# Kernel optimization log

Measured on AMD Instinct MI355X. Metric: run time of the kernel, lower is better.

The kernel has to match this reference:

```python
import jax, jax.numpy as jnp
import numpy as np

D_MODEL = 1024
N_HEADS = 16
D_K = D_MODEL // N_HEADS


def setup_inputs() -> dict:
    key = jax.random.key(0)
    ks = jax.random.split(key, 9)
    B, L = 2, 2048
    s = 1.0 / np.sqrt(D_MODEL)
    return {
        "x": jax.random.normal(ks[0], (B, L, D_MODEL), dtype=jnp.float32),
        "Wq": jax.random.normal(ks[1], (D_MODEL, D_MODEL), dtype=jnp.float32) * s,
        "bq": jnp.zeros((D_MODEL,), dtype=jnp.float32),
        "Wk": jax.random.normal(ks[2], (D_MODEL, D_MODEL), dtype=jnp.float32) * s,
        "bk": jnp.zeros((D_MODEL,), dtype=jnp.float32),
        "Wv": jax.random.normal(ks[3], (D_MODEL, D_MODEL), dtype=jnp.float32) * s,
        "bv": jnp.zeros((D_MODEL,), dtype=jnp.float32),
        "Wo": jax.random.normal(ks[4], (D_MODEL, D_MODEL), dtype=jnp.float32) * s,
        "bo": jnp.zeros((D_MODEL,), dtype=jnp.float32),
    }


def reference(x, Wq, bq, Wk, bk, Wv, bv, Wo, bo):
    B, L, D = x.shape
    H, dk = N_HEADS, D_K
    # torch Linear: y = x @ W.T + b
    def proj(W, b):
        y = jnp.einsum('bld,ed->ble', x, W) + b
        return y.reshape(B, L, H, dk).transpose(0, 2, 1, 3)  # [B,H,L,dk]
    Q = proj(Wq, bq)
    K = proj(Wk, bk)
    V = proj(Wv, bv)
    scores = jnp.einsum('bhqd,bhkd->bhqk', Q, K) / jnp.sqrt(jnp.float32(dk))
    probs = jax.nn.softmax(scores, axis=-1)
    # intervention: zero column 0, then average with original -> halve column 0
    col_scale = jnp.where(jnp.arange(L) == 0, 0.5, 1.0).astype(probs.dtype)
    combined = probs * col_scale  # broadcast over last axis
    out = jnp.einsum('bhqk,bhkd->bhqd', combined, V)
    out = out.transpose(0, 2, 1, 3).reshape(B, L, D)
    # dropout in eval mode = identity
    return jnp.einsum('bld,ed->ble', out, Wo) + bo
```

## Files before the change

kernel.cpp:

```cpp
#include <hip/hip_runtime.h>
#include <stdint.h>

#define DMODEL 1024
#define LSEQ   2048
#define NBATCH 2
#define NHEADS 16
#define DKH    64
#define MROWS  4096
#define KSPLIT 2

typedef __attribute__((ext_vector_type(8))) short short8;
typedef __attribute__((ext_vector_type(4))) float f32x4;
typedef __attribute__((ext_vector_type(16))) float f32x16;
typedef __attribute__((ext_vector_type(2))) int int2v;

__device__ __forceinline__ unsigned short f2b(float f) {
  union { float f; unsigned int u; } v; v.f = f;
  unsigned int r = v.u + 0x7FFFu + ((v.u >> 16) & 1u);
  return (unsigned short)(r >> 16);
}

__device__ __forceinline__ float b2f(unsigned short u) {
  union { unsigned int i; float f; } v; v.i = ((unsigned int)u) << 16; return v.f;
}

__device__ __forceinline__ unsigned int cvtpk(float lo, float hi) {
  unsigned int r;
  asm volatile("v_cvt_pk_bf16_f32 %0, %1, %2" : "=v"(r) : "v"(lo), "v"(hi));
  return r;
}

__device__ __forceinline__ int2v pl32swap(unsigned int a, unsigned int b) {
  return __builtin_amdgcn_permlane32_swap((int)a, (int)b, false, false);
}

__device__ __forceinline__ void async16(const void* g, void* l) {
  __builtin_amdgcn_global_load_lds(
      (const __attribute__((address_space(1))) unsigned int*)g,
      (__attribute__((address_space(3))) unsigned int*)l, 16, 0, 0);
}

__global__ void k_cvt(const float* __restrict__ s, unsigned short* __restrict__ d, int n4) {
  int i = blockIdx.x * blockDim.x + threadIdx.x;
  if (i >= n4) return;
  float4 v = ((const float4*)s)[i];
  ushort4 o;
  o.x = f2b(v.x); o.y = f2b(v.y); o.z = f2b(v.z); o.w = f2b(v.w);
  ((ushort4*)d)[i] = o;
}

__global__ void k_cvtw(const float* __restrict__ s0, const float* __restrict__ s1,
                       const float* __restrict__ s2, const float* __restrict__ s3,
                       unsigned short* __restrict__ d0, unsigned short* __restrict__ d1,
                       unsigned short* __restrict__ d2, unsigned short* __restrict__ d3) {
  const float* s; unsigned short* d;
  switch (blockIdx.y) {
    case 0: s = s0; d = d0; break;
    case 1: s = s1; d = d1; break;
    case 2: s = s2; d = d2; break;
    default: s = s3; d = d3; break;
  }
  int i = blockIdx.x * blockDim.x + threadIdx.x;
  float4 v = ((const float4*)s)[i];
  ushort4 o;
  o.x = f2b(v.x); o.y = f2b(v.y); o.z = f2b(v.z); o.w = f2b(v.w);
  ((ushort4*)d)[i] = o;
}

__device__ __forceinline__ void gemm_mainloop(
    const unsigned short* __restrict__ A, const unsigned short* __restrict__ B,
    int rowBase, int colBase, char* As, char* Bs, f32x4 acc[4][4])
{
  const int tid  = threadIdx.x;
  const int lane = tid & 63;
  const int wr   = tid >> 7;
  const int wc   = (tid >> 6) & 1;
  for (int kt = 0; kt < DMODEL / 64; ++kt) {
    const int k0 = kt * 64;
    __syncthreads();
#pragma unroll
    for (int p = 0; p < 4; ++p) {
      const int chunk = p * 256 + tid;
      const int row   = chunk >> 3;
      const int cs    = (chunk & 7) ^ (row & 7);
      async16(A + (size_t)(rowBase + row) * DMODEL + k0 + cs * 8,
              As + (p * 256 + (tid & 0xC0)) * 16);
      async16(B + (size_t)(colBase + row) * DMODEL + k0 + cs * 8,
              Bs + (p * 256 + (tid & 0xC0)) * 16);
    }
    __syncthreads();
#pragma unroll
    for (int ks = 0; ks < 2; ++ks) {
      short8 af[4], bfr[4];
#pragma unroll
      for (int m = 0; m < 4; ++m) {
        const int ra = wr * 64 + m * 16 + (lane & 15);
        af[m]  = *(const short8*)(As + ra * 128 + (((ks * 4 + (lane >> 4)) ^ (ra & 7)) * 16));
        const int rb = wc * 64 + m * 16 + (lane & 15);
        bfr[m] = *(const short8*)(Bs + rb * 128 + (((ks * 4 + (lane >> 4)) ^ (rb & 7)) * 16));
      }
#pragma unroll
      for (int m = 0; m < 4; ++m)
#pragma unroll
        for (int n = 0; n < 4; ++n)
          acc[m][n] = __builtin_amdgcn_mfma_f32_16x16x32_bf16(af[m], bfr[n], acc[m][n], 0, 0, 0);
    }
  }
}

__global__ __launch_bounds__(256, 2) void k_gemm_qkv(
    const unsigned short* __restrict__ xb,
    const unsigned short* __restrict__ Wqb, const unsigned short* __restrict__ Wkb,
    const unsigned short* __restrict__ Wvb,
    const float* __restrict__ bq, const float* __restrict__ bk, const float* __restrict__ bv,
    unsigned short* __restrict__ Q, unsigned short* __restrict__ Ksw,
    unsigned short* __restrict__ Vsw)
{
  __shared__ char As[16384];
  __shared__ char Bs[16384];
  const int z = blockIdx.z;
  const unsigned short* W = (z == 0) ? Wqb : ((z == 1) ? Wkb : Wvb);
  const float* bias       = (z == 0) ? bq  : ((z == 1) ? bk  : bv);
  const int rowBase = blockIdx.x * 128, colBase = blockIdx.y * 128;

  f32x4 zero = {0.f, 0.f, 0.f, 0.f};
  f32x4 acc[4][4];
#pragma unroll
  for (int m = 0; m < 4; ++m)
#pragma unroll
    for (int n = 0; n < 4; ++n) acc[m][n] = zero;

  gemm_mainloop(xb, W, rowBase, colBase, As, Bs, acc);

  const int tid = threadIdx.x, lane = tid & 63;
  const int wr = tid >> 7, wc = (tid >> 6) & 1;
  const float scale = (z == 0) ? 0.18033688011112042f : 1.0f;
#pragma unroll
  for (int m = 0; m < 4; ++m) {
#pragma unroll
    for (int n = 0; n < 4; ++n) {
      const int gcol = colBase + wc * 64 + n * 16 + (lane & 15);
      const float bb = bias[gcol];
      const int h = gcol >> 6, d = gcol & 63;
      if (z == 0) {
#pragma unroll
        for (int r = 0; r < 4; ++r) {
          const int grow = rowBase + wr * 64 + m * 16 + ((lane >> 4) << 2) + r;
          const int bi = grow >> 11, l = grow & 2047;
          Q[(((size_t)(bi * NHEADS + h)) * LSEQ + l) * DKH + d] =
              f2b((acc[m][n][r] + bb) * scale);
        }
      } else if (z == 1) {
#pragma unroll
        for (int r = 0; r < 4; ++r) {
          const int grow = rowBase + wr * 64 + m * 16 + ((lane >> 4) << 2) + r;
          const int bi = grow >> 11, l = grow & 2047;
          const int bh = bi * NHEADS + h;
          Ksw[(size_t)(bh * 32 + (l >> 6)) * 4096 + ((d >> 3) * 64 + (l & 63)) * 8 + (d & 7)] =
              f2b(acc[m][n][r] + bb);
        }
      } else {
        const int grow0 = rowBase + wr * 64 + m * 16 + ((lane >> 4) << 2);
        const int bi = grow0 >> 11, l0 = grow0 & 2047;
        const int bh = bi * NHEADS + h;
        ushort4 o;
        o.x = f2b(acc[m][n][0] + bb);
        o.y = f2b(acc[m][n][1] + bb);
        o.z = f2b(acc[m][n][2] + bb);
        o.w = f2b(acc[m][n][3] + bb);
        *(ushort4*)(Vsw + (size_t)(bh * 32 + (l0 >> 6)) * 4096 +
                    (((l0 & 63) >> 3) * 64 + d) * 8 + (l0 & 7)) = o;
      }
    }
  }
}

__global__ __launch_bounds__(256, 4) void k_attn(
    const unsigned short* __restrict__ Q, const unsigned short* __restrict__ Ksw,
    const unsigned short* __restrict__ Vsw,
    unsigned short* __restrict__ Op0, unsigned short* __restrict__ Op1,
    float* __restrict__ Lp)
{
  __shared__ char Ks[2][8192];
  __shared__ char Vs[2][8192];

  const int tid = threadIdx.x, lane = tid & 63, w = tid >> 6;
  const int hi = lane >> 5;
  const int ql = lane & 31;

  const int flat = blockIdx.x;
  const int g  = flat & 63;
  const int qi = flat >> 6;
  const int bh = g >> 1, ks = g & 1;
  const int b = bh >> 4, h = bh & 15;
  const int q0 = qi * 128 + w * 32;

  unsigned short* __restrict__ Op = ks ? Op1 : Op0;
  const unsigned short* __restrict__ Qh = Q + (size_t)bh * LSEQ * DKH;

  short8 qf[4];
#pragma unroll
  for (int c = 0; c < 4; ++c)
    qf[c] = *(const short8*)(Qh + (size_t)(q0 + ql) * DKH + c * 16 + hi * 8);

  union { unsigned short u[8]; short8 v; } ones;
#pragma unroll
  for (int j = 0; j < 8; ++j) ones.u[j] = 0x3F80;

  f32x16 oacc[2], lacc, z16;
#pragma unroll
  for (int r = 0; r < 16; ++r) {
    oacc[0][r] = 0.f; oacc[1][r] = 0.f; lacc[r] = 0.f; z16[r] = 0.f;
  }
  float p0 = 0.f;

  auto stage = [&](int buf, int kt2) {
    const unsigned short* Kt = Ksw + (size_t)(bh * 32 + kt2) * 4096;
    const unsigned short* Vt = Vsw + (size_t)(bh * 32 + kt2) * 4096;
#pragma unroll
    for (int p = 0; p < 2; ++p) {
      const int c = p * 256 + tid;
      async16(Kt + c * 8, Ks[buf] + (p * 256 + (tid & 0xC0)) * 16);
      async16(Vt + c * 8, Vs[buf] + (p * 256 + (tid & 0xC0)) * 16);
    }
  };

  const int t0 = ks * (LSEQ / 64 / KSPLIT);
  const int NT = LSEQ / 64 / KSPLIT;

  stage(0, t0);
  __syncthreads();

  int cur = 0;
  for (int it = 0; it < NT; ++it) {
    if (it < NT - 1) stage(cur ^ 1, t0 + it + 1);
    const char* Kc = Ks[cur];
    const char* Vc = Vs[cur];

    f32x16 sv[2];
#pragma unroll
    for (int b2 = 0; b2 < 2; ++b2) {
      short8 kf = *(const short8*)(Kc + ((0 * 2 + hi) * 64 + b2 * 32 + ql) * 16);
      sv[b2] = __builtin_amdgcn_mfma_f32_32x32x16_bf16(kf, qf[0], z16, 0, 0, 0);
    }
#pragma unroll
    for (int c = 1; c < 4; ++c) {
#pragma unroll
      for (int b2 = 0; b2 < 2; ++b2) {
        short8 kf = *(const short8*)(Kc + ((c * 2 + hi) * 64 + b2 * 32 + ql) * 16);
        sv[b2] = __builtin_amdgcn_mfma_f32_32x32x16_bf16(kf, qf[c], sv[b2], 0, 0, 0);
      }
    }

#pragma unroll
    for (int b2 = 0; b2 < 2; ++b2)
#pragma unroll
      for (int r = 0; r < 16; ++r) sv[b2][r] = __builtin_amdgcn_exp2f(sv[b2][r]);

    if (ks == 0 && it == 0 && hi == 0) { p0 = sv[0][0]; sv[0][0] *= 0.5f; }

    unsigned int pk[2][4][2];
#pragma unroll
    for (int b2 = 0; b2 < 2; ++b2)
#pragma unroll
      for (int R = 0; R < 4; ++R) {
        pk[b2][R][0] = cvtpk(sv[b2][4 * R + 0], sv[b2][4 * R + 1]);
        pk[b2][R][1] = cvtpk(sv[b2][4 * R + 2], sv[b2][4 * R + 3]);
      }

#pragma unroll
    for (int kc = 0; kc < 4; ++kc) {
      const int b2 = kc >> 1, Rl = 2 * (kc & 1);
      int2v sw0 = pl32swap(pk[b2][Rl][0], pk[b2][Rl + 1][0]);
      int2v sw1 = pl32swap(pk[b2][Rl][1], pk[b2][Rl + 1][1]);
      union { int i[4]; short8 v; } pa;
      pa.i[0] = sw0[0]; pa.i[1] = sw1[0]; pa.i[2] = sw0[1]; pa.i[3] = sw1[1];
      lacc = __builtin_amdgcn_mfma_f32_32x32x16_bf16(pa.v, ones.v, lacc, 0, 0, 0);
#pragma unroll
      for (int n = 0; n < 2; ++n) {
        short8 vb = *(const short8*)(Vc + ((kc * 2 + hi) * 64 + n * 32 + ql) * 16);
        oacc[n] = __builtin_amdgcn_mfma_f32_32x32x16_bf16(pa.v, vb, oacc[n], 0, 0, 0);
      }
    }

    __syncthreads();
    cur ^= 1;
  }

#pragma unroll
  for (int r = 0; r < 16; ++r) {
    const int qrow = (r & 3) + 8 * (r >> 2) + 4 * hi;
    float lv = lacc[r];
    if (ks == 0) lv += 0.5f * __shfl(p0, qrow);
#pragma unroll
    for (int n = 0; n < 2; ++n) {
      Op[(size_t)(b * LSEQ + q0 + qrow) * DMODEL + h * 64 + n * 32 + ql] =
          f2b(oacc[n][r]);
    }
    if (ql == 0)
      Lp[ks * (32 * LSEQ) + bh * LSEQ + q0 + qrow] = lv;
  }
}

__global__ void k_combine(const unsigned short* __restrict__ o0,
                          const unsigned short* __restrict__ o1,
                          const float* __restrict__ Lp,
                          unsigned short* __restrict__ AO)
{
  const int i = blockIdx.x * blockDim.x + threadIdx.x;
  const int row = i >> 7;
  const int q = row & 2047, b = row >> 11;
  const int h = (i & 127) >> 3;
  const int bhq = (b * 16 + h) * 2048 + q;
  const float inv = 1.0f / (Lp[bhq] + Lp[32 * LSEQ + bhq]);
  short8 a = ((const short8*)o0)[i];
  short8 c = ((const short8*)o1)[i];
  union { unsigned short u[8]; short8 v; } o;
#pragma unroll
  for (int j = 0; j < 8; ++j)
    o.u[j] = f2b((b2f((unsigned short)a[j]) + b2f((unsigned short)c[j])) * inv);
  ((short8*)AO)[i] = o.v;
}

__global__ __launch_bounds__(256, 2) void k_gemm_out(
    const unsigned short* __restrict__ AO, const unsigned short* __restrict__ Wob,
    const float* __restrict__ bo, float* __restrict__ out)
{
  __shared__ char As[16384];
  __shared__ char Bs[16384];
  const int rowBase = blockIdx.x * 128, colBase = blockIdx.y * 128;
  f32x4 zero = {0.f, 0.f, 0.f, 0.f};
  f32x4 acc[4][4];
#pragma unroll
  for (int m = 0; m < 4; ++m)
#pragma unroll
    for (int n = 0; n < 4; ++n) acc[m][n] = zero;

  gemm_mainloop(AO, Wob, rowBase, colBase, As, Bs, acc);

  const int tid = threadIdx.x, lane = tid & 63;
  const int wr = tid >> 7, wc = (tid >> 6) & 1;
#pragma unroll
  for (int m = 0; m < 4; ++m) {
#pragma unroll
    for (int n = 0; n < 4; ++n) {
      const int gcol = colBase + wc * 64 + n * 16 + (lane & 15);
      const float bb = bo[gcol];
#pragma unroll
      for (int r = 0; r < 4; ++r) {
        const int grow = rowBase + wr * 64 + m * 16 + ((lane >> 4) << 2) + r;
        out[(size_t)grow * DMODEL + gcol] = acc[m][n][r] + bb;
      }
    }
  }
}

extern "C" void kernel_launch(void* const* d_in, const int* in_sizes, int n_in,
                              void* d_out, int out_size, void* d_ws, size_t ws_size,
                              hipStream_t stream) {
  const float* x  = (const float*)d_in[0];
  const float* Wq = (const float*)d_in[1];
  const float* bq = (const float*)d_in[2];
  const float* Wk = (const float*)d_in[3];
  const float* bk = (const float*)d_in[4];
  const float* Wv = (const float*)d_in[5];
  const float* bv = (const float*)d_in[6];
  const float* Wo = (const float*)d_in[7];
  const float* bo = (const float*)d_in[8];
  float* out = (float*)d_out;
  char* ws = (char*)d_ws;

  const size_t MB = 1u << 20;
  unsigned short* xb  = (unsigned short*)(ws);
  unsigned short* Wob = (unsigned short*)(ws + 8  * MB);
  unsigned short* Wqb = (unsigned short*)(ws + 10 * MB);
  unsigned short* Wkb = (unsigned short*)(ws + 12 * MB);
  unsigned short* Wvb = (unsigned short*)(ws + 14 * MB);
  unsigned short* Qb  = (unsigned short*)(ws + 16 * MB);
  unsigned short* Ksw = (unsigned short*)(ws + 24 * MB);
  unsigned short* Vsw = (unsigned short*)(ws + 32 * MB);
  unsigned short* AOb = (unsigned short*)(ws + 40 * MB);
  unsigned short* Op0 = (unsigned short*)(ws);
  unsigned short* Op1 = (unsigned short*)(ws + 48 * MB);
  float*          Lpp = (float*)(ws + 56 * MB);

  k_cvt<<<4096, 256, 0, stream>>>(x, xb, MROWS * DMODEL / 4);
  dim3 gw(DMODEL * DMODEL / 4 / 256, 4);
  k_cvtw<<<gw, 256, 0, stream>>>(Wq, Wk, Wv, Wo, Wqb, Wkb, Wvb, Wob);

  dim3 gqkv(MROWS / 128, DMODEL / 128, 3);
  k_gemm_qkv<<<gqkv, 256, 0, stream>>>(xb, Wqb, Wkb, Wvb, bq, bk, bv, Qb, Ksw, Vsw);

  k_attn<<<16 * 32 * KSPLIT, 256, 0, stream>>>(Qb, Ksw, Vsw, Op0, Op1, Lpp);

  k_combine<<<2048, 256, 0, stream>>>(Op0, Op1, Lpp, AOb);

  dim3 gout(MROWS / 128, DMODEL / 128);
  k_gemm_out<<<gout, 256, 0, stream>>>(AOb, Wob, bo, out);
}
```

Baseline: 117.7 us.

## Software-pipeline attention: overlap QK^T of next tile with PV of previous tile

The attention loop is restructured so each iteration computes scores for tile i while running the P·V and row-sum MFMAs for tile i-1, with V held in a triple buffer and K in a double buffer. The aim is to hide the exp and convert/permlane latency behind independent MFMA work. The x and weight fp32-to-bf16 conversions are also merged into one launch to save a kernel launch. In exchange the kernel keeps more registers live (the packed probabilities) and uses extra LDS for the third V buffer, which may reduce occupancy.

Result: no change. 115.6 us (-1.8%).

```diff
diff --git a/kernel.cpp b/kernel.cpp
--- a/kernel.cpp
+++ b/kernel.cpp
@@ -40,27 +40,23 @@
       (__attribute__((address_space(3))) unsigned int*)l, 16, 0, 0);
 }
 
-__global__ void k_cvt(const float* __restrict__ s, unsigned short* __restrict__ d, int n4) {
-  int i = blockIdx.x * blockDim.x + threadIdx.x;
-  if (i >= n4) return;
-  float4 v = ((const float4*)s)[i];
-  ushort4 o;
-  o.x = f2b(v.x); o.y = f2b(v.y); o.z = f2b(v.z); o.w = f2b(v.w);
-  ((ushort4*)d)[i] = o;
-}
-
-__global__ void k_cvtw(const float* __restrict__ s0, const float* __restrict__ s1,
-                       const float* __restrict__ s2, const float* __restrict__ s3,
-                       unsigned short* __restrict__ d0, unsigned short* __restrict__ d1,
-                       unsigned short* __restrict__ d2, unsigned short* __restrict__ d3) {
+__global__ void k_cvtall(const float* __restrict__ x,
+                         const float* __restrict__ w0, const float* __restrict__ w1,
+                         const float* __restrict__ w2, const float* __restrict__ w3,
+                         unsigned short* __restrict__ xb,
+                         unsigned short* __restrict__ d0, unsigned short* __restrict__ d1,
+                         unsigned short* __restrict__ d2, unsigned short* __restrict__ d3) {
+  const int y = blockIdx.y;
   const float* s; unsigned short* d;
-  switch (blockIdx.y) {
-    case 0: s = s0; d = d0; break;
-    case 1: s = s1; d = d1; break;
-    case 2: s = s2; d = d2; break;
-    default: s = s3; d = d3; break;
-  }
-  int i = blockIdx.x * blockDim.x + threadIdx.x;
+  switch (y) {
+    case 0: case 1: case 2: case 3:
+      s = x + (size_t)y * 1048576; d = xb + (size_t)y * 1048576; break;
+    case 4: s = w0; d = d0; break;
+    case 5: s = w1; d = d1; break;
+    case 6: s = w2; d = d2; break;
+    default: s = w3; d = d3; break;
+  }
+  const int i = blockIdx.x * blockDim.x + threadIdx.x;
   float4 v = ((const float4*)s)[i];
   ushort4 o;
   o.x = f2b(v.x); o.y = f2b(v.y); o.z = f2b(v.z); o.w = f2b(v.w);
@@ -182,11 +178,12 @@
     float* __restrict__ Lp)
 {
   __shared__ char Ks[2][8192];
-  __shared__ char Vs[2][8192];
-
-  const int tid = threadIdx.x, lane = tid & 63, w = tid >> 6;
+  __shared__ char Vs[3][8192];
+
+  const int tid = threadIdx.x, lane = tid & 63;
   const int hi = lane >> 5;
   const int ql = lane & 31;
+  const int w = tid >> 6;
 
   const int flat = blockIdx.x;
   const int g  = flat & 63;
@@ -214,51 +211,47 @@
   }
   float p0 = 0.f;
 
-  auto stage = [&](int buf, int kt2) {
-    const unsigned short* Kt = Ksw + (size_t)(bh * 32 + kt2) * 4096;
-    const unsigned short* Vt = Vsw + (size_t)(bh * 32 + kt2) * 4096;
+  auto stageK = [&](int slot, int t2) {
+    const unsigned short* Kt = Ksw + (size_t)(bh * 32 + t2) * 4096;
 #pragma unroll
     for (int p = 0; p < 2; ++p) {
       const int c = p * 256 + tid;
-      async16(Kt + c * 8, Ks[buf] + (p * 256 + (tid & 0xC0)) * 16);
-      async16(Vt + c * 8, Vs[buf] + (p * 256 + (tid & 0xC0)) * 16);
+      async16(Kt + c * 8, Ks[slot] + (p * 256 + (tid & 0xC0)) * 16);
+    }
+  };
+  auto stageV = [&](int slot, int t2) {
+    const unsigned short* Vt = Vsw + (size_t)(bh * 32 + t2) * 4096;
+#pragma unroll
+    for (int p = 0; p < 2; ++p) {
+      const int c = p * 256 + tid;
+      async16(Vt + c * 8, Vs[slot] + (p * 256 + (tid & 0xC0)) * 16);
     }
   };
 
   const int t0 = ks * (LSEQ / 64 / KSPLIT);
   const int NT = LSEQ / 64 / KSPLIT;
 
-  stage(0, t0);
+  stageK(0, t0); stageV(0, t0);
   __syncthreads();
 
-  int cur = 0;
-  for (int it = 0; it < NT; ++it) {
-    if (it < NT - 1) stage(cur ^ 1, t0 + it + 1);
-    const char* Kc = Ks[cur];
-    const char* Vc = Vs[cur];
-
+  short8 paP[4];
+
+  {
+    stageK(1, t0 + 1); stageV(1, t0 + 1);
+    const char* Kc = Ks[0];
     f32x16 sv[2];
 #pragma unroll
-    for (int b2 = 0; b2 < 2; ++b2) {
-      short8 kf = *(const short8*)(Kc + ((0 * 2 + hi) * 64 + b2 * 32 + ql) * 16);
-      sv[b2] = __builtin_amdgcn_mfma_f32_32x32x16_bf16(kf, qf[0], z16, 0, 0, 0);
-    }
-#pragma unroll
-    for (int c = 1; c < 4; ++c) {
-#pragma unroll
-      for (int b2 = 0; b2 < 2; ++b2) {
-        short8 kf = *(const short8*)(Kc + ((c * 2 + hi) * 64 + b2 * 32 + ql) * 16);
-        sv[b2] = __builtin_amdgcn_mfma_f32_32x32x16_bf16(kf, qf[c], sv[b2], 0, 0, 0);
-      }
-    }
-
+    for (int c = 0; c < 4; ++c) {
+      short8 kf0 = *(const short8*)(Kc + ((c * 2 + hi) * 64 + ql) * 16);
+      short8 kf1 = *(const short8*)(Kc + ((c * 2 + hi) * 64 + 32 + ql) * 16);
+      sv[0] = __builtin_amdgcn_mfma_f32_32x32x16_bf16(kf0, qf[c], c ? sv[0] : z16, 0, 0, 0);
+      sv[1] = __builtin_amdgcn_mfma_f32_32x32x16_bf16(kf1, qf[c], c ? sv[1] : z16, 0, 0, 0);
+    }
 #pragma unroll
     for (int b2 = 0; b2 < 2; ++b2)
 #pragma unroll
       for (int r = 0; r < 16; ++r) sv[b2][r] = __builtin_amdgcn_exp2f(sv[b2][r]);
-
-    if (ks == 0 && it == 0 && hi == 0) { p0 = sv[0][0]; sv[0][0] *= 0.5f; }
-
+    if (ks == 0 && hi == 0) { p0 = sv[0][0]; sv[0][0] *= 0.5f; }
     unsigned int pk[2][4][2];
 #pragma unroll
     for (int b2 = 0; b2 < 2; ++b2)
@@ -267,7 +260,6 @@
         pk[b2][R][0] = cvtpk(sv[b2][4 * R + 0], sv[b2][4 * R + 1]);
         pk[b2][R][1] = cvtpk(sv[b2][4 * R + 2], sv[b2][4 * R + 3]);
       }
-
 #pragma unroll
     for (int kc = 0; kc < 4; ++kc) {
       const int b2 = kc >> 1, Rl = 2 * (kc & 1);
@@ -275,16 +267,64 @@
       int2v sw1 = pl32swap(pk[b2][Rl][1], pk[b2][Rl + 1][1]);
       union { int i[4]; short8 v; } pa;
       pa.i[0] = sw0[0]; pa.i[1] = sw1[0]; pa.i[2] = sw0[1]; pa.i[3] = sw1[1];
-      lacc = __builtin_amdgcn_mfma_f32_32x32x16_bf16(pa.v, ones.v, lacc, 0, 0, 0);
-#pragma unroll
-      for (int n = 0; n < 2; ++n) {
-        short8 vb = *(const short8*)(Vc + ((kc * 2 + hi) * 64 + n * 32 + ql) * 16);
-        oacc[n] = __builtin_amdgcn_mfma_f32_32x32x16_bf16(pa.v, vb, oacc[n], 0, 0, 0);
+      paP[kc] = pa.v;
+    }
+    __syncthreads();
+  }
+
+  for (int i = 1; i < NT; ++i) {
+    if (i < NT - 1) { stageK((i + 1) & 1, t0 + i + 1); stageV((i + 1) % 3, t0 + i + 1); }
+    const char* Kc = Ks[i & 1];
+    const char* Vp = Vs[(i - 1) % 3];
+
+    f32x16 sv[2];
+#pragma unroll
+    for (int s = 0; s < 4; ++s) {
+      short8 kf0 = *(const short8*)(Kc + ((s * 2 + hi) * 64 + ql) * 16);
+      short8 kf1 = *(const short8*)(Kc + ((s * 2 + hi) * 64 + 32 + ql) * 16);
+      sv[0] = __builtin_amdgcn_mfma_f32_32x32x16_bf16(kf0, qf[s], s ? sv[0] : z16, 0, 0, 0);
+      sv[1] = __builtin_amdgcn_mfma_f32_32x32x16_bf16(kf1, qf[s], s ? sv[1] : z16, 0, 0, 0);
+      lacc = __builtin_amdgcn_mfma_f32_32x32x16_bf16(paP[s], ones.v, lacc, 0, 0, 0);
+      short8 vb0 = *(const short8*)(Vp + ((s * 2 + hi) * 64 + ql) * 16);
+      short8 vb1 = *(const short8*)(Vp + ((s * 2 + hi) * 64 + 32 + ql) * 16);
+      oacc[0] = __builtin_amdgcn_mfma_f32_32x32x16_bf16(paP[s], vb0, oacc[0], 0, 0, 0);
+      oacc[1] = __builtin_amdgcn_mfma_f32_32x32x16_bf16(paP[s], vb1, oacc[1], 0, 0, 0);
+    }
+
+#pragma unroll
+    for (int b2 = 0; b2 < 2; ++b2)
+#pragma unroll
+      for (int r = 0; r < 16; ++r) sv[b2][r] = __builtin_amdgcn_exp2f(sv[b2][r]);
+    unsigned int pk[2][4][2];
+#pragma unroll
+    for (int b2 = 0; b2 < 2; ++b2)
+#pragma unroll
+      for (int R = 0; R < 4; ++R) {
+        pk[b2][R][0] = cvtpk(sv[b2][4 * R + 0], sv[b2][4 * R + 1]);
+        pk[b2][R][1] = cvtpk(sv[b2][4 * R + 2], sv[b2][4 * R + 3]);
       }
-    }
-
+#pragma unroll
+    for (int kc = 0; kc < 4; ++kc) {
+      const int b2 = kc >> 1, Rl = 2 * (kc & 1);
+      int2v sw0 = pl32swap(pk[b2][Rl][0], pk[b2][Rl + 1][0]);
+      int2v sw1 = pl32swap(pk[b2][Rl][1], pk[b2][Rl + 1][1]);
+      union { int i[4]; short8 v; } pa;
+      pa.i[0] = sw0[0]; pa.i[1] = sw1[0]; pa.i[2] = sw0[1]; pa.i[3] = sw1[1];
+      paP[kc] = pa.v;
+    }
     __syncthreads();
-    cur ^= 1;
+  }
+
+  {
+    const char* Vp = Vs[(NT - 1) % 3];
+#pragma unroll
+    for (int s = 0; s < 4; ++s) {
+      lacc = __builtin_amdgcn_mfma_f32_32x32x16_bf16(paP[s], ones.v, lacc, 0, 0, 0);
+      short8 vb0 = *(const short8*)(Vp + ((s * 2 + hi) * 64 + ql) * 16);
+      short8 vb1 = *(const short8*)(Vp + ((s * 2 + hi) * 64 + 32 + ql) * 16);
+      oacc[0] = __builtin_amdgcn_mfma_f32_32x32x16_bf16(paP[s], vb0, oacc[0], 0, 0, 0);
+      oacc[1] = __builtin_amdgcn_mfma_f32_32x32x16_bf16(paP[s], vb1, oacc[1], 0, 0, 0);
+    }
   }
 
 #pragma unroll
@@ -384,9 +424,8 @@
   unsigned short* Op1 = (unsigned short*)(ws + 48 * MB);
   float*          Lpp = (float*)(ws + 56 * MB);
 
-  k_cvt<<<4096, 256, 0, stream>>>(x, xb, MROWS * DMODEL / 4);
-  dim3 gw(DMODEL * DMODEL / 4 / 256, 4);
-  k_cvtw<<<gw, 256, 0, stream>>>(Wq, Wk, Wv, Wo, Wqb, Wkb, Wvb, Wob);
+  dim3 gcv(1024, 8);
+  k_cvtall<<<gcv, 256, 0, stream>>>(x, Wq, Wk, Wv, Wo, xb, Wqb, Wkb, Wvb, Wob);
 
   dim3 gqkv(MROWS / 128, DMODEL / 128, 3);
   k_gemm_qkv<<<gqkv, 256, 0, stream>>>(xb, Wqb, Wkb, Wvb, bq, bk, bv, Qb, Ksw, Vsw);
```

## Load K/V fragments directly into registers and merge conversion kernels

Applied to the files above, without the earlier changes.

The attention kernel no longer stages K and V tiles through double-buffered LDS with async copies and block barriers. Each lane now loads its MFMA fragments straight from global memory into registers and prefetches the next tile's K and V while the current tile is computed. The launch bound drops to 2 blocks per SM to make room for the extra registers. Separately, the x and weight bf16 conversion kernels are merged into one launch to save launch overhead. The trade-off is lower occupancy and redundant global/L2 reads, since the four waves in a block each read the same K/V tile instead of sharing it through LDS.

Result: no change. 117.1 us (-0.5%).

```diff
diff --git a/kernel.cpp b/kernel.cpp
--- a/kernel.cpp
+++ b/kernel.cpp
@@ -40,27 +40,23 @@
       (__attribute__((address_space(3))) unsigned int*)l, 16, 0, 0);
 }
 
-__global__ void k_cvt(const float* __restrict__ s, unsigned short* __restrict__ d, int n4) {
-  int i = blockIdx.x * blockDim.x + threadIdx.x;
-  if (i >= n4) return;
-  float4 v = ((const float4*)s)[i];
-  ushort4 o;
-  o.x = f2b(v.x); o.y = f2b(v.y); o.z = f2b(v.z); o.w = f2b(v.w);
-  ((ushort4*)d)[i] = o;
-}
-
-__global__ void k_cvtw(const float* __restrict__ s0, const float* __restrict__ s1,
-                       const float* __restrict__ s2, const float* __restrict__ s3,
-                       unsigned short* __restrict__ d0, unsigned short* __restrict__ d1,
-                       unsigned short* __restrict__ d2, unsigned short* __restrict__ d3) {
+__global__ void k_cvtall(const float* __restrict__ x,
+                         const float* __restrict__ w0, const float* __restrict__ w1,
+                         const float* __restrict__ w2, const float* __restrict__ w3,
+                         unsigned short* __restrict__ xb,
+                         unsigned short* __restrict__ d0, unsigned short* __restrict__ d1,
+                         unsigned short* __restrict__ d2, unsigned short* __restrict__ d3) {
+  const int y = blockIdx.y;
   const float* s; unsigned short* d;
-  switch (blockIdx.y) {
-    case 0: s = s0; d = d0; break;
-    case 1: s = s1; d = d1; break;
-    case 2: s = s2; d = d2; break;
-    default: s = s3; d = d3; break;
-  }
-  int i = blockIdx.x * blockDim.x + threadIdx.x;
+  switch (y) {
+    case 0: case 1: case 2: case 3:
+      s = x + (size_t)y * 1048576; d = xb + (size_t)y * 1048576; break;
+    case 4: s = w0; d = d0; break;
+    case 5: s = w1; d = d1; break;
+    case 6: s = w2; d = d2; break;
+    default: s = w3; d = d3; break;
+  }
+  const int i = blockIdx.x * blockDim.x + threadIdx.x;
   float4 v = ((const float4*)s)[i];
   ushort4 o;
   o.x = f2b(v.x); o.y = f2b(v.y); o.z = f2b(v.z); o.w = f2b(v.w);
@@ -175,18 +171,16 @@
   }
 }
 
-__global__ __launch_bounds__(256, 4) void k_attn(
+__global__ __launch_bounds__(256, 2) void k_attn(
     const unsigned short* __restrict__ Q, const unsigned short* __restrict__ Ksw,
     const unsigned short* __restrict__ Vsw,
     unsigned short* __restrict__ Op0, unsigned short* __restrict__ Op1,
     float* __restrict__ Lp)
 {
-  __shared__ char Ks[2][8192];
-  __shared__ char Vs[2][8192];
-
-  const int tid = threadIdx.x, lane = tid & 63, w = tid >> 6;
+  const int tid = threadIdx.x, lane = tid & 63;
   const int hi = lane >> 5;
   const int ql = lane & 31;
+  const int w = tid >> 6;
 
   const int flat = blockIdx.x;
   const int g  = flat & 63;
@@ -214,42 +208,43 @@
   }
   float p0 = 0.f;
 
-  auto stage = [&](int buf, int kt2) {
-    const unsigned short* Kt = Ksw + (size_t)(bh * 32 + kt2) * 4096;
-    const unsigned short* Vt = Vsw + (size_t)(bh * 32 + kt2) * 4096;
-#pragma unroll
-    for (int p = 0; p < 2; ++p) {
-      const int c = p * 256 + tid;
-      async16(Kt + c * 8, Ks[buf] + (p * 256 + (tid & 0xC0)) * 16);
-      async16(Vt + c * 8, Vs[buf] + (p * 256 + (tid & 0xC0)) * 16);
-    }
-  };
-
   const int t0 = ks * (LSEQ / 64 / KSPLIT);
   const int NT = LSEQ / 64 / KSPLIT;
 
-  stage(0, t0);
-  __syncthreads();
-
-  int cur = 0;
-  for (int it = 0; it < NT; ++it) {
-    if (it < NT - 1) stage(cur ^ 1, t0 + it + 1);
-    const char* Kc = Ks[cur];
-    const char* Vc = Vs[cur];
+  const int lv = hi * 512 + ql * 8;
+#define FOFF(c, b2) ((c) * 1024 + (b2) * 256 + lv)
+
+  const unsigned short* Kt = Ksw + (size_t)(bh * 32 + t0) * 4096;
+  const unsigned short* Vt = Vsw + (size_t)(bh * 32 + t0) * 4096;
+
+  short8 kreg[8], vreg[8];
+#pragma unroll
+  for (int c = 0; c < 4; ++c)
+#pragma unroll
+    for (int b2 = 0; b2 < 2; ++b2) {
+      kreg[c * 2 + b2] = *(const short8*)(Kt + FOFF(c, b2));
+      vreg[c * 2 + b2] = *(const short8*)(Vt + FOFF(c, b2));
+    }
+
+  for (int i = 0; i < NT; ++i) {
+    const unsigned short* Kn = Ksw + (size_t)(bh * 32 + t0 + i + 1) * 4096;
+    const unsigned short* Vn = Vsw + (size_t)(bh * 32 + t0 + i + 1) * 4096;
 
     f32x16 sv[2];
 #pragma unroll
-    for (int b2 = 0; b2 < 2; ++b2) {
-      short8 kf = *(const short8*)(Kc + ((0 * 2 + hi) * 64 + b2 * 32 + ql) * 16);
-      sv[b2] = __builtin_amdgcn_mfma_f32_32x32x16_bf16(kf, qf[0], z16, 0, 0, 0);
-    }
-#pragma unroll
-    for (int c = 1; c < 4; ++c) {
-#pragma unroll
-      for (int b2 = 0; b2 < 2; ++b2) {
-        short8 kf = *(const short8*)(Kc + ((c * 2 + hi) * 64 + b2 * 32 + ql) * 16);
-        sv[b2] = __builtin_amdgcn_mfma_f32_32x32x16_bf16(kf, qf[c], sv[b2], 0, 0, 0);
-      }
+    for (int c = 0; c < 4; ++c) {
+      sv[0] = __builtin_amdgcn_mfma_f32_32x32x16_bf16(kreg[c * 2 + 0], qf[c],
+                                                      c ? sv[0] : z16, 0, 0, 0);
+      sv[1] = __builtin_amdgcn_mfma_f32_32x32x16_bf16(kreg[c * 2 + 1], qf[c],
+                                                      c ? sv[1] : z16, 0, 0, 0);
+    }
+
+    if (i < NT - 1) {
+#pragma unroll
+      for (int c = 0; c < 4; ++c)
+#pragma unroll
+        for (int b2 = 0; b2 < 2; ++b2)
+          kreg[c * 2 + b2] = *(const short8*)(Kn + FOFF(c, b2));
     }
 
 #pragma unroll
@@ -257,7 +252,7 @@
 #pragma unroll
       for (int r = 0; r < 16; ++r) sv[b2][r] = __builtin_amdgcn_exp2f(sv[b2][r]);
 
-    if (ks == 0 && it == 0 && hi == 0) { p0 = sv[0][0]; sv[0][0] *= 0.5f; }
+    if (ks == 0 && i == 0 && hi == 0) { p0 = sv[0][0]; sv[0][0] *= 0.5f; }
 
     unsigned int pk[2][4][2];
 #pragma unroll
@@ -276,29 +271,32 @@
       union { int i[4]; short8 v; } pa;
       pa.i[0] = sw0[0]; pa.i[1] = sw1[0]; pa.i[2] = sw0[1]; pa.i[3] = sw1[1];
       lacc = __builtin_amdgcn_mfma_f32_32x32x16_bf16(pa.v, ones.v, lacc, 0, 0, 0);
-#pragma unroll
-      for (int n = 0; n < 2; ++n) {
-        short8 vb = *(const short8*)(Vc + ((kc * 2 + hi) * 64 + n * 32 + ql) * 16);
-        oacc[n] = __builtin_amdgcn_mfma_f32_32x32x16_bf16(pa.v, vb, oacc[n], 0, 0, 0);
-      }
-    }
-
-    __syncthreads();
-    cur ^= 1;
-  }
+      oacc[0] = __builtin_amdgcn_mfma_f32_32x32x16_bf16(pa.v, vreg[kc * 2 + 0], oacc[0], 0, 0, 0);
+      oacc[1] = __builtin_amdgcn_mfma_f32_32x32x16_bf16(pa.v, vreg[kc * 2 + 1], oacc[1], 0, 0, 0);
+    }
+
+    if (i < NT - 1) {
+#pragma unroll
+      for (int c = 0; c < 4; ++c)
+#pragma unroll
+        for (int b2 = 0; b2 < 2; ++b2)
+          vreg[c * 2 + b2] = *(const short8*)(Vn + FOFF(c, b2));
+    }
+  }
+#undef FOFF
 
 #pragma unroll
   for (int r = 0; r < 16; ++r) {
     const int qrow = (r & 3) + 8 * (r >> 2) + 4 * hi;
-    float lv = lacc[r];
-    if (ks == 0) lv += 0.5f * __shfl(p0, qrow);
+    float lv2 = lacc[r];
+    if (ks == 0) lv2 += 0.5f * __shfl(p0, qrow);
 #pragma unroll
     for (int n = 0; n < 2; ++n) {
       Op[(size_t)(b * LSEQ + q0 + qrow) * DMODEL + h * 64 + n * 32 + ql] =
           f2b(oacc[n][r]);
     }
     if (ql == 0)
-      Lp[ks * (32 * LSEQ) + bh * LSEQ + q0 + qrow] = lv;
+      Lp[ks * (32 * LSEQ) + bh * LSEQ + q0 + qrow] = lv2;
   }
 }
 
@@ -384,9 +382,8 @@
   unsigned short* Op1 = (unsigned short*)(ws + 48 * MB);
   float*          Lpp = (float*)(ws + 56 * MB);
 
-  k_cvt<<<4096, 256, 0, stream>>>(x, xb, MROWS * DMODEL / 4);
-  dim3 gw(DMODEL * DMODEL / 4 / 256, 4);
-  k_cvtw<<<gw, 256, 0, stream>>>(Wq, Wk, Wv, Wo, Wqb, Wkb, Wvb, Wob);
+  dim3 gcv(1024, 8);
+  k_cvtall<<<gcv, 256, 0, stream>>>(x, Wq, Wk, Wv, Wo, xb, Wqb, Wkb, Wvb, Wob);
 
   dim3 gqkv(MROWS / 128, DMODEL / 128, 3);
   k_gemm_qkv<<<gqkv, 256, 0, stream>>>(xb, Wqb, Wkb, Wvb, bq, bk, bv, Qb, Ksw, Vsw);
```

## Fuse split-K attention combine into output GEMM A-load and merge conversion kernels

Applied to the files above, without the earlier changes.

The split-K combine (sum of two partial outputs scaled by the inverse of the summed row sums) moves into the A-tile load of the output projection GEMM, so the AO intermediate and one kernel launch go away. The x and weight conversion kernels become a single launch. In exchange, the A tile is now loaded synchronously through registers with extra arithmetic and a division per row, and each A element is recomputed by all 8 column blocks instead of once. This may slow the GEMM mainloop, which no longer uses async loads for A.

After: 132.8 us. 12.8% more time.

```diff
diff --git a/kernel.cpp b/kernel.cpp
--- a/kernel.cpp
+++ b/kernel.cpp
@@ -40,27 +40,23 @@
       (__attribute__((address_space(3))) unsigned int*)l, 16, 0, 0);
 }
 
-__global__ void k_cvt(const float* __restrict__ s, unsigned short* __restrict__ d, int n4) {
-  int i = blockIdx.x * blockDim.x + threadIdx.x;
-  if (i >= n4) return;
-  float4 v = ((const float4*)s)[i];
-  ushort4 o;
-  o.x = f2b(v.x); o.y = f2b(v.y); o.z = f2b(v.z); o.w = f2b(v.w);
-  ((ushort4*)d)[i] = o;
-}
-
-__global__ void k_cvtw(const float* __restrict__ s0, const float* __restrict__ s1,
-                       const float* __restrict__ s2, const float* __restrict__ s3,
-                       unsigned short* __restrict__ d0, unsigned short* __restrict__ d1,
-                       unsigned short* __restrict__ d2, unsigned short* __restrict__ d3) {
+__global__ void k_cvtall(const float* __restrict__ x,
+                         const float* __restrict__ w0, const float* __restrict__ w1,
+                         const float* __restrict__ w2, const float* __restrict__ w3,
+                         unsigned short* __restrict__ xb,
+                         unsigned short* __restrict__ d0, unsigned short* __restrict__ d1,
+                         unsigned short* __restrict__ d2, unsigned short* __restrict__ d3) {
+  const int y = blockIdx.y;
   const float* s; unsigned short* d;
-  switch (blockIdx.y) {
-    case 0: s = s0; d = d0; break;
-    case 1: s = s1; d = d1; break;
-    case 2: s = s2; d = d2; break;
-    default: s = s3; d = d3; break;
-  }
-  int i = blockIdx.x * blockDim.x + threadIdx.x;
+  switch (y) {
+    case 0: case 1: case 2: case 3:
+      s = x + (size_t)y * 1048576; d = xb + (size_t)y * 1048576; break;
+    case 4: s = w0; d = d0; break;
+    case 5: s = w1; d = d1; break;
+    case 6: s = w2; d = d2; break;
+    default: s = w3; d = d3; break;
+  }
+  const int i = blockIdx.x * blockDim.x + threadIdx.x;
   float4 v = ((const float4*)s)[i];
   ushort4 o;
   o.x = f2b(v.x); o.y = f2b(v.y); o.z = f2b(v.z); o.w = f2b(v.w);
@@ -302,33 +298,19 @@
   }
 }
 
-__global__ void k_combine(const unsigned short* __restrict__ o0,
-                          const unsigned short* __restrict__ o1,
-                          const float* __restrict__ Lp,
-                          unsigned short* __restrict__ AO)
-{
-  const int i = blockIdx.x * blockDim.x + threadIdx.x;
-  const int row = i >> 7;
-  const int q = row & 2047, b = row >> 11;
-  const int h = (i & 127) >> 3;
-  const int bhq = (b * 16 + h) * 2048 + q;
-  const float inv = 1.0f / (Lp[bhq] + Lp[32 * LSEQ + bhq]);
-  short8 a = ((const short8*)o0)[i];
-  short8 c = ((const short8*)o1)[i];
-  union { unsigned short u[8]; short8 v; } o;
-#pragma unroll
-  for (int j = 0; j < 8; ++j)
-    o.u[j] = f2b((b2f((unsigned short)a[j]) + b2f((unsigned short)c[j])) * inv);
-  ((short8*)AO)[i] = o.v;
-}
-
 __global__ __launch_bounds__(256, 2) void k_gemm_out(
-    const unsigned short* __restrict__ AO, const unsigned short* __restrict__ Wob,
+    const unsigned short* __restrict__ Op0, const unsigned short* __restrict__ Op1,
+    const float* __restrict__ Lp, const unsigned short* __restrict__ Wob,
     const float* __restrict__ bo, float* __restrict__ out)
 {
   __shared__ char As[16384];
   __shared__ char Bs[16384];
   const int rowBase = blockIdx.x * 128, colBase = blockIdx.y * 128;
+  const int tid  = threadIdx.x;
+  const int lane = tid & 63;
+  const int wr   = tid >> 7;
+  const int wc   = (tid >> 6) & 1;
+
   f32x4 zero = {0.f, 0.f, 0.f, 0.f};
   f32x4 acc[4][4];
 #pragma unroll
@@ -336,10 +318,48 @@
 #pragma unroll
     for (int n = 0; n < 4; ++n) acc[m][n] = zero;
 
-  gemm_mainloop(AO, Wob, rowBase, colBase, As, Bs, acc);
-
-  const int tid = threadIdx.x, lane = tid & 63;
-  const int wr = tid >> 7, wc = (tid >> 6) & 1;
+  for (int kt = 0; kt < DMODEL / 64; ++kt) {
+    const int k0 = kt * 64;
+    __syncthreads();
+#pragma unroll
+    for (int p = 0; p < 4; ++p) {
+      const int chunk = p * 256 + tid;
+      const int row   = chunk >> 3;
+      const int cs    = (chunk & 7) ^ (row & 7);
+      const int grow  = rowBase + row;
+      const int bi  = grow >> 11, q = grow & 2047;
+      const int bhq = (bi * NHEADS + kt) * LSEQ + q;
+      const float invl = 1.0f / (Lp[bhq] + Lp[32 * LSEQ + bhq]);
+      const size_t src = (size_t)grow * DMODEL + k0 + cs * 8;
+      short8 a0 = *(const short8*)(Op0 + src);
+      short8 a1 = *(const short8*)(Op1 + src);
+      union { unsigned short u[8]; short8 v; } o;
+#pragma unroll
+      for (int j = 0; j < 8; ++j)
+        o.u[j] = f2b((b2f((unsigned short)a0[j]) + b2f((unsigned short)a1[j])) * invl);
+      *(short8*)(As + chunk * 16) = o.v;
+      async16(Wob + (size_t)(colBase + row) * DMODEL + k0 + cs * 8,
+              Bs + (p * 256 + (tid & 0xC0)) * 16);
+    }
+    __syncthreads();
+#pragma unroll
+    for (int ks = 0; ks < 2; ++ks) {
+      short8 af[4], bfr[4];
+#pragma unroll
+      for (int m = 0; m < 4; ++m) {
+        const int ra = wr * 64 + m * 16 + (lane & 15);
+        af[m]  = *(const short8*)(As + ra * 128 + (((ks * 4 + (lane >> 4)) ^ (ra & 7)) * 16));
+        const int rb = wc * 64 + m * 16 + (lane & 15);
+        bfr[m] = *(const short8*)(Bs + rb * 128 + (((ks * 4 + (lane >> 4)) ^ (rb & 7)) * 16));
+      }
+#pragma unroll
+      for (int m = 0; m < 4; ++m)
+#pragma unroll
+        for (int n = 0; n < 4; ++n)
+          acc[m][n] = __builtin_amdgcn_mfma_f32_16x16x32_bf16(af[m], bfr[n], acc[m][n], 0, 0, 0);
+    }
+  }
+
 #pragma unroll
   for (int m = 0; m < 4; ++m) {
 #pragma unroll
@@ -379,22 +399,18 @@
   unsigned short* Qb  = (unsigned short*)(ws + 16 * MB);
   unsigned short* Ksw = (unsigned short*)(ws + 24 * MB);
   unsigned short* Vsw = (unsigned short*)(ws + 32 * MB);
-  unsigned short* AOb = (unsigned short*)(ws + 40 * MB);
   unsigned short* Op0 = (unsigned short*)(ws);
   unsigned short* Op1 = (unsigned short*)(ws + 48 * MB);
   float*          Lpp = (float*)(ws + 56 * MB);
 
-  k_cvt<<<4096, 256, 0, stream>>>(x, xb, MROWS * DMODEL / 4);
-  dim3 gw(DMODEL * DMODEL / 4 / 256, 4);
-  k_cvtw<<<gw, 256, 0, stream>>>(Wq, Wk, Wv, Wo, Wqb, Wkb, Wvb, Wob);
+  dim3 gcv(1024, 8);
+  k_cvtall<<<gcv, 256, 0, stream>>>(x, Wq, Wk, Wv, Wo, xb, Wqb, Wkb, Wvb, Wob);
 
   dim3 gqkv(MROWS / 128, DMODEL / 128, 3);
   k_gemm_qkv<<<gqkv, 256, 0, stream>>>(xb, Wqb, Wkb, Wvb, bq, bk, bv, Qb, Ksw, Vsw);
 
   k_attn<<<16 * 32 * KSPLIT, 256, 0, stream>>>(Qb, Ksw, Vsw, Op0, Op1, Lpp);
 
-  k_combine<<<2048, 256, 0, stream>>>(Op0, Op1, Lpp, AOb);
-
   dim3 gout(MROWS / 128, DMODEL / 128);
-  k_gemm_out<<<gout, 256, 0, stream>>>(AOb, Wob, bo, out);
-}
+  k_gemm_out<<<gout, 256, 0, stream>>>(Op0, Op1, Lpp, Wob, bo, out);
+}
```
